# Optimization experiments

Measured on AMD Instinct MI355X. Metric: run time of the kernel, lower is better.

## Reference

```python
import jax, jax.numpy as jnp
import numpy as np
import math

B, C_IN, S, E, H, DFF = 8, 16, 1024, 128, 8, 512
DH = E // H
EPS_BN = 1e-5
EPS_LN = 1e-5


def _tape_pe(d_model, seq_len):
    pos = jnp.arange(seq_len, dtype=jnp.float32)[:, None]
    div = jnp.exp(jnp.arange(0, d_model, 2, dtype=jnp.float32) * (-math.log(10000.0) / d_model))
    ang = pos * div * (d_model / seq_len)
    pe = jnp.zeros((seq_len, d_model), dtype=jnp.float32)
    pe = pe.at[:, 0::2].set(jnp.sin(ang))
    pe = pe.at[:, 1::2].set(jnp.cos(ang))
    return pe  # [S, E]


def _ln(x, g, b, eps=EPS_LN):
    m = jnp.mean(x, axis=-1, keepdims=True)
    v = jnp.mean((x - m) ** 2, axis=-1, keepdims=True)
    return (x - m) / jnp.sqrt(v + eps) * g + b


def _bn(x, g, b, mean, var, eps=EPS_BN):
    # eval-mode BatchNorm2d over channel axis 1 of NCHW
    sh = (1, -1, 1, 1)
    return (x - mean.reshape(sh)) / jnp.sqrt(var.reshape(sh) + eps) * g.reshape(sh) + b.reshape(sh)


def setup_inputs() -> dict:
    key = jax.random.key(0)
    ks = jax.random.split(key, 24)
    f = lambda k, shape, s=0.05: (jax.random.normal(k, shape, dtype=jnp.float32) * s)
    inp = {
        'x': jax.random.normal(ks[0], (B, C_IN, S), dtype=jnp.float32),
        'conv1_w': f(ks[1], (E * 4, 1, 1, 7)),
        'conv1_b': f(ks[2], (E * 4,)),
        'bn1_g': 1.0 + f(ks[3], (E * 4,)),
        'bn1_b': f(ks[4], (E * 4,)),
        'bn1_m': jnp.zeros((E * 4,), jnp.float32),
        'bn1_v': jnp.ones((E * 4,), jnp.float32),
        'conv2_w': f(ks[5], (E, E * 4, C_IN, 1)),
        'conv2_b': f(ks[6], (E,)),
        'bn2_g': 1.0 + f(ks[7], (E,)),
        'bn2_b': f(ks[8], (E,)),
        'bn2_m': jnp.zeros((E,), jnp.float32),
        'bn2_v': jnp.ones((E,), jnp.float32),
        'wq': f(ks[9], (E, E)),
        'wk': f(ks[10], (E, E)),
        'wv': f(ks[11], (E, E)),
        'rel_bias_table': f(ks[12], (2 * S - 1, H), 0.02),
        'ln_attn_g': jnp.ones((E,), jnp.float32),
        'ln_attn_b': jnp.zeros((E,), jnp.float32),
        'ln1_g': jnp.ones((E,), jnp.float32),
        'ln1_b': jnp.zeros((E,), jnp.float32),
        'ln2_g': jnp.ones((E,), jnp.float32),
        'ln2_b': jnp.zeros((E,), jnp.float32),
        'ff_w1': f(ks[13], (DFF, E)),
        'ff_b1': f(ks[14], (DFF,)),
        'ff_w2': f(ks[15], (E, DFF)),
        'ff_b2': f(ks[16], (E,)),
    }
    return inp


def reference(x, conv1_w, conv1_b, bn1_g, bn1_b, bn1_m, bn1_v,
              conv2_w, conv2_b, bn2_g, bn2_b, bn2_m, bn2_v,
              wq, wk, wv, rel_bias_table,
              ln_attn_g, ln_attn_b, ln1_g, ln1_b, ln2_g, ln2_b,
              ff_w1, ff_b1, ff_w2, ff_b2):
    dn = ('NCHW', 'OIHW', 'NCHW')
    # conv stem: x [B, C_in, S] -> [B, 1, C_in, S]
    h = x[:, None, :, :]
    h = jax.lax.conv_general_dilated(h, conv1_w, (1, 1), [(0, 0), (3, 3)], dimension_numbers=dn)
    h = h + conv1_b[None, :, None, None]
    h = jax.nn.gelu(_bn(h, bn1_g, bn1_b, bn1_m, bn1_v), approximate=False)
    h = jax.lax.conv_general_dilated(h, conv2_w, (1, 1), [(0, 0), (0, 0)], dimension_numbers=dn)
    h = h + conv2_b[None, :, None, None]
    h = jax.nn.gelu(_bn(h, bn2_g, bn2_b, bn2_m, bn2_v), approximate=False)
    x_src = jnp.transpose(h[:, :, 0, :], (0, 2, 1))  # [B, S, E]

    # tAPE absolute positional encoding
    x_pos = x_src + _tape_pe(E, S)[None]

    # Attention_Rel_Scl (eRPE): bias added AFTER softmax, as in the original
    scale = E ** (-0.5)
    q = jnp.einsum('bsd,ed->bse', x_pos, wq).reshape(B, S, H, DH).transpose(0, 2, 1, 3)
    k = jnp.einsum('bsd,ed->bse', x_pos, wk).reshape(B, S, H, DH).transpose(0, 2, 1, 3)
    v = jnp.einsum('bsd,ed->bse', x_pos, wv).reshape(B, S, H, DH).transpose(0, 2, 1, 3)
    attn = jax.nn.softmax(jnp.einsum('bhid,bhjd->bhij', q, k) * scale, axis=-1)
    idx = jnp.arange(S)[:, None] - jnp.arange(S)[None, :] + (S - 1)  # [S, S]
    rel_bias = rel_bias_table[idx].transpose(2, 0, 1)[None]  # [1, H, S, S]
    attn = attn + rel_bias
    out = jnp.einsum('bhij,bhjd->bhid', attn, v).transpose(0, 2, 1, 3).reshape(B, S, E)
    out = _ln(out, ln_attn_g, ln_attn_b)

    att = _ln(x_src + out, ln1_g, ln1_b)
    ff = jnp.maximum(jnp.einsum('bsd,fd->bsf', att, ff_w1) + ff_b1, 0.0)
    ff = jnp.einsum('bsf,ef->bse', ff, ff_w2) + ff_b2
    y = _ln(att + ff, ln2_g, ln2_b)
    return jnp.transpose(y, (0, 2, 1))  # [B, E, S]
```

## Files before the change

kernel.cpp:

```cpp
#include <hip/hip_runtime.h>
#include <math.h>

#define BB    8
#define CIN   16
#define SS    1024
#define EE    128
#define HH    8
#define DHH   16
#define O1    512
#define DFFN  512
#define K2TOT 8192

#define PE_OFF    0
#define BN1SC_OFF 131072
#define BN1SH_OFF 131584
#define BN2SC_OFF 132096
#define BN2SH_OFF 132224
#define W1P_OFF   133120
#define WQKV_BF_OFF 135168
#define W1FF_BF_OFF 159744
#define W2FF_BF_OFF 192512
#define XSRC_OFF  262144
#define Q_OFF     1310720
#define KK_OFF    2359296
#define V_OFF     3407872
#define ATTN_OFF  4456448
#define ATT_OFF   5505024
#define FFH_OFF   6553600
#define W2CONV_BF_OFF 8650752

typedef __attribute__((ext_vector_type(8))) short short8;
typedef __attribute__((ext_vector_type(8))) unsigned short ushort8;
typedef __attribute__((ext_vector_type(4))) unsigned short us4;
typedef __attribute__((ext_vector_type(4))) float f32x4;
typedef _Float16 f16_t;
typedef __attribute__((ext_vector_type(4))) _Float16 half4;
typedef __attribute__((ext_vector_type(8))) _Float16 half8;

__device__ __forceinline__ float wave_sum(float v) {
    #pragma unroll
    for (int o = 32; o > 0; o >>= 1) v += __shfl_xor(v, o);
    return v;
}

__device__ __forceinline__ float gelu_exact(float x) {
    return 0.5f * x * (1.0f + erff(x * 0.7071067811865476f));
}

__device__ __forceinline__ float gelu_tanh(float x) {
    float x2 = x * x;
    float y = x * fmaf(0.0713548162f, x2, 1.5957691216f);
    float E = __expf(y);
    float r = __builtin_amdgcn_rcpf(E + 1.0f);
    return fmaf(-x, r, x);
}

__device__ __forceinline__ unsigned short f2bf(float f) {
    unsigned int u = __float_as_uint(f);
    unsigned int r = u + 0x7FFFu + ((u >> 16) & 1u);
    return (unsigned short)(r >> 16);
}

__device__ __forceinline__ float bf2f(unsigned short u) {
    return __uint_as_float(((unsigned int)u) << 16);
}

__device__ __forceinline__ void castw_body(const float* __restrict__ src,
                                           unsigned short* __restrict__ dst, int K, int tid) {
    int g = tid & 7, e = (tid >> 3) & 127, rest = tid >> 10;
    int KB = K >> 6;
    int kb = rest % KB, nb = rest / KB;
    int col = nb * 128 + e;
    const float* s = src + (size_t)col * K + kb * 64 + ((g ^ (e & 7)) << 3);
    ushort8 v;
    #pragma unroll
    for (int j = 0; j < 8; j++) v[j] = f2bf(s[j]);
    *(ushort8*)&dst[(size_t)tid << 3] = v;
}

__global__ __launch_bounds__(256) void k0_all(const float* __restrict__ conv1_w,
                                              const float* __restrict__ conv1_b,
                                              const float* __restrict__ bn1_g,
                                              const float* __restrict__ bn1_b,
                                              const float* __restrict__ bn1_m,
                                              const float* __restrict__ bn1_v,
                                              const float* __restrict__ conv2_w,
                                              const float* __restrict__ conv2_b,
                                              const float* __restrict__ bn2_g,
                                              const float* __restrict__ bn2_b,
                                              const float* __restrict__ bn2_m,
                                              const float* __restrict__ bn2_v,
                                              const float* __restrict__ wq,
                                              const float* __restrict__ wk,
                                              const float* __restrict__ wv,
                                              const float* __restrict__ ff_w1,
                                              const float* __restrict__ ff_w2,
                                              float* __restrict__ ws) {
    int bid = blockIdx.x, t = threadIdx.x;
    if (bid < 512) {
        int idx = bid * 256 + t;
        int s = idx >> 7, e = idx & 127;
        int i = e >> 1;
        float freq = expf((float)(2 * i) * (-9.210340371976184f / 128.0f));
        float ang = (float)s * freq * 0.125f;
        ws[PE_OFF + idx] = (e & 1) ? cosf(ang) : sinf(ang);
    } else if (bid < 515) {
        int u = (bid - 512) * 256 + t;
        if (u < 512) {
            float sc = bn1_g[u] * rsqrtf(bn1_v[u] + 1e-5f);
            ws[BN1SC_OFF + u] = sc;
            ws[BN1SH_OFF + u] = (conv1_b[u] - bn1_m[u]) * sc + bn1_b[u];
        } else if (u < 640) {
            int e = u - 512;
            float sc = bn2_g[e] * rsqrtf(bn2_v[e] + 1e-5f);
            ws[BN2SC_OFF + e] = sc;
            ws[BN2SH_OFF + e] = (conv2_b[e] - bn2_m[e]) * sc + bn2_b[e];
        }
    } else if (bid < 1027) {
        castw_body(conv2_w, (unsigned short*)(ws + W2CONV_BF_OFF), 8192, (bid - 515) * 256 + t);
    } else if (bid < 1035) {
        castw_body(wq, (unsigned short*)(ws + WQKV_BF_OFF), 128, (bid - 1027) * 256 + t);
    } else if (bid < 1043) {
        castw_body(wk, (unsigned short*)(ws + WQKV_BF_OFF) + 16384, 128, (bid - 1035) * 256 + t);
    } else if (bid < 1051) {
        castw_body(wv, (unsigned short*)(ws + WQKV_BF_OFF) + 32768, 128, (bid - 1043) * 256 + t);
    } else if (bid < 1083) {
        castw_body(ff_w1, (unsigned short*)(ws + W1FF_BF_OFF), 128, (bid - 1051) * 256 + t);
    } else if (bid < 1115) {
        castw_body(ff_w2, (unsigned short*)(ws + W2FF_BF_OFF), 512, (bid - 1083) * 256 + t);
    } else {
        unsigned short* w1p = (unsigned short*)(ws + W1P_OFF);
        for (int id = t; id < 4096; id += 256) {
            int o = id >> 3, u = id & 7;
            float sc = bn1_g[o] * rsqrtf(bn1_v[o] + 1e-5f);
            float v = (u < 7) ? conv1_w[o * 7 + u] * sc : 0.f;
            w1p[id] = f2bf(v);
        }
    }
}

__global__ __launch_bounds__(256, 3) void k1_mfma(const float* __restrict__ x,
                                                  float* __restrict__ ws) {
    __shared__ float xt[CIN][40];
    __shared__ unsigned short w1ps[256 * 8];
    __shared__ float sh1s[256];
    __shared__ unsigned short Ab[2][32 * 64];

    const int t = threadIdx.x;
    const int wave = t >> 6, lane = t & 63;
    const int row0 = blockIdx.x * 32;
    const int ksplit = blockIdx.y;
    const int b = row0 >> 10, s0 = row0 & 1023;
    const int obase = ksplit * 256;

    for (int i = t; i < CIN * 38; i += 256) {
        int c = i / 38, j = i % 38;
        int gs = s0 + j - 3;
        xt[c][j] = (gs >= 0 && gs < SS) ? x[(b * CIN + c) * SS + gs] : 0.f;
    }
    {
        const ushort8* w1pg = (const ushort8*)((const unsigned short*)(ws + W1P_OFF)) + obase;
        if (t < 256) *(ushort8*)&w1ps[t << 3] = w1pg[t];
        if (t < 256) sh1s[t] = ws[BN1SH_OFF + obase + t];
    }
    __syncthreads();

    const char* w2g = (const char*)(ws + W2CONV_BF_OFF);
    const int wr = wave >> 1, wc = wave & 1;
    const int lrow = lane & 15, lq = lane >> 4;

    int boff[8];
    #pragma unroll
    for (int ks2 = 0; ks2 < 2; ++ks2) {
        int G = (ks2 << 2) + lq;
        #pragma unroll
        for (int nf = 0; nf < 4; ++nf) {
            int e = (wc << 6) + (nf << 4) + lrow;
            boff[ks2 * 4 + nf] = (e << 7) + ((G ^ (e & 7)) << 4);
        }
    }

    auto loadB = [&](int kbl, short8 (&dst)[8]) {
        const char* g = w2g + ((size_t)(ksplit * 64 + kbl) << 14);
        #pragma unroll
        for (int i = 0; i < 8; ++i)
            dst[i] = *(const short8*)(g + boff[i]);
    };

    const int c_ = lane & 15;
    float xv[14];
    #pragma unroll
    for (int j = 0; j < 14; j++) xv[j] = xt[c_][(wave << 3) + j];
    int wbase[8];
    #pragma unroll
    for (int i = 0; i < 8; i++) {
        int ss = (wave << 3) + i;
        wbase[i] = (ss << 6) + ((((lane >> 3) ^ (ss & 7))) << 3) + (lane & 7);
    }

    auto computeH1 = [&](int kbl, int buf) {
        int ol = (kbl << 2) + (lane >> 4);
        ushort8 wv8 = *(const ushort8*)&w1ps[ol << 3];
        float w0 = bf2f(wv8[0]), w1_ = bf2f(wv8[1]), w2_ = bf2f(wv8[2]), w3 = bf2f(wv8[3]);
        float w4 = bf2f(wv8[4]), w5 = bf2f(wv8[5]), w6 = bf2f(wv8[6]);
        float sh = sh1s[ol];
        unsigned short* abf = &Ab[buf][0];
        #pragma unroll
        for (int i = 0; i < 8; i++) {
            float p = xv[i]   * w0 + xv[i+1] * w1_ + xv[i+2] * w2_ + xv[i+3] * w3
                    + xv[i+4] * w4 + xv[i+5] * w5 + xv[i+6] * w6;
            abf[wbase[i]] = f2bf(gelu_tanh(p + sh));
        }
    };

    f32x4 acc[4];
    #pragma unroll
    for (int i = 0; i < 4; i++) acc[i] = (f32x4){0.f, 0.f, 0.f, 0.f};

    auto mfmaPhase = [&](short8 (&bb)[8], int buf) {
        #pragma unroll
        for (int ks2 = 0; ks2 < 2; ++ks2) {
            int G = (ks2 << 2) + lq;
            int arow = (wr << 4) + lrow;
            short8 a = *(const short8*)&Ab[buf][(arow << 6) + ((G ^ (arow & 7)) << 3)];
            #pragma unroll
            for (int nf = 0; nf < 4; ++nf)
                acc[nf] = __builtin_amdgcn_mfma_f32_16x16x32_bf16(a, bb[ks2 * 4 + nf], acc[nf], 0, 0, 0);
        }
    };

    short8 bA[8], bB[8];
    loadB(0, bA);
    computeH1(0, 0);
    __syncthreads();
    for (int kb2 = 0; kb2 < 64; kb2 += 2) {
        loadB(kb2 + 1, bB);
        mfmaPhase(bA, 0);
        computeH1(kb2 + 1, 1);
        __syncthreads();
        if (kb2 + 2 < 64) loadB(kb2 + 2, bA);
        mfmaPhase(bB, 1);
        if (kb2 + 2 < 64) {
            computeH1(kb2 + 2, 0);
            __syncthreads();
        }
    }

    float* P = ws + FFH_OFF + (size_t)ksplit * 1048576;
    #pragma unroll
    for (int nf = 0; nf < 4; ++nf) {
        int e = (wc << 6) + (nf << 4) + lrow;
        #pragma unroll
        for (int r = 0; r < 4; ++r) {
            int srow = s0 + (wr << 4) + (lq << 2) + r;
            P[(((size_t)(b * SS + srow)) << 7) + e] = acc[nf][r];
        }
    }
}

__global__ __launch_bounds__(256) void k1b_combine(float* __restrict__ ws) {
    int f = (blockIdx.x * 256 + threadIdx.x) * 4;
    int e0 = f & 127;
    float4 p0 = *(const float4*)&ws[FFH_OFF + f];
    float4 p1 = *(const float4*)&ws[FFH_OFF + 1048576 + f];
    float4 sc = *(const float4*)&ws[BN2SC_OFF + e0];
    float4 sh = *(const float4*)&ws[BN2SH_OFF + e0];
    float4 o;
    o.x = gelu_exact(fmaf(p0.x + p1.x, sc.x, sh.x));
    o.y = gelu_exact(fmaf(p0.y + p1.y, sc.y, sh.y));
    o.z = gelu_exact(fmaf(p0.z + p1.z, sc.z, sh.z));
    o.w = gelu_exact(fmaf(p0.w + p1.w, sc.w, sh.w));
    *(float4*)&ws[XSRC_OFF + f] = o;
}

__global__ __launch_bounds__(256) void k2_mfma(float* __restrict__ ws) {
    __shared__ unsigned short As[32 * 128];
    __shared__ unsigned short Bs[128 * 128];
    __shared__ float ys[32][132];
    const int t = threadIdx.x;
    const int rt = blockIdx.x, mat = blockIdx.y;
    const int wave = t >> 6, lane = t & 63;

    const char* bg = (const char*)((const unsigned short*)(ws + WQKV_BF_OFF) + mat * 16384);
    #pragma unroll
    for (int c8 = 0; c8 < 8; ++c8) {
        int off = c8 * 4096 + wave * 1024;
        __builtin_amdgcn_global_load_lds(
            (const __attribute__((address_space(1))) unsigned int*)(bg + off + lane * 16),
            (__attribute__((address_space(3))) unsigned int*)(&Bs[off >> 1]), 16, 0, 0);
    }
    const int bs0 = rt * 32;
    const int sl0 = bs0 & 1023;
    for (int i = t; i < 1024; i += 256) {
        int row = i >> 5, d0 = (i & 31) << 2;
        float4 xvv = *(const float4*)&ws[XSRC_OFF + (size_t)(bs0 + row) * EE + d0];
        float4 pv = *(const float4*)&ws[PE_OFF + (size_t)(sl0 + row) * EE + d0];
        us4 o;
        o[0] = f2bf(xvv.x + pv.x); o[1] = f2bf(xvv.y + pv.y);
        o[2] = f2bf(xvv.z + pv.z); o[3] = f2bf(xvv.w + pv.w);
        int slot = (d0 >> 3) ^ (row & 7);
        *(us4*)&As[(row << 7) + (slot << 3) + (d0 & 7)] = o;
    }
    __syncthreads();

    const int wr = wave >> 1, wc = wave & 1;
    const int lrow = lane & 15, lq = lane >> 4;
    f32x4 acc[4];
    #pragma unroll
    for (int i = 0; i < 4; i++) acc[i] = (f32x4){0.f, 0.f, 0.f, 0.f};

    #pragma unroll
    for (int ksname = 0; ksname < 4; ++ksname) {
        int G = (ksname << 2) + lq;
        int arow = (wr << 4) + lrow;
        short8 a = *(const short8*)&As[(arow << 7) + ((G ^ (arow & 7)) << 3)];
        #pragma unroll
        for (int nf = 0; nf < 4; ++nf) {
            int e = (wc << 6) + (nf << 4) + lrow;
            short8 bf = *(const short8*)&Bs[((G >> 3) << 13) + (e << 6) + (((G & 7) ^ (e & 7)) << 3)];
            acc[nf] = __builtin_amdgcn_mfma_f32_16x16x32_bf16(a, bf, acc[nf], 0, 0, 0);
        }
    }

    #pragma unroll
    for (int nf = 0; nf < 4; ++nf) {
        int e = (wc << 6) + (nf << 4) + lrow;
        #pragma unroll
        for (int r = 0; r < 4; ++r)
            ys[(wr << 4) + (lq << 2) + r][e] = acc[nf][r];
    }
    __syncthreads();

    const int b = bs0 >> 10;
    if (mat <= 1) {
        int row = t >> 3, h8 = t & 7;
        float scl = (mat == 0) ? 0.08838834764831845f : 1.0f;
        f16_t* dst = (f16_t*)(ws + (mat == 0 ? Q_OFF : KK_OFF))
                   + (((size_t)(b * HH + h8)) * SS + (sl0 + row)) * DHH;
        half8 v0, v1;
        #pragma unroll
        for (int d = 0; d < 8; d++) v0[d] = (f16_t)(ys[row][h8 * 16 + d] * scl);
        #pragma unroll
        for (int d = 0; d < 8; d++) v1[d] = (f16_t)(ys[row][h8 * 16 + 8 + d] * scl);
        *(half8*)&dst[0] = v0;
        *(half8*)&dst[8] = v1;
    } else {
        int c = t & 127, hf = t >> 7;
        int h8 = c >> 4, d2 = c & 15;
        f16_t* dst = (f16_t*)(ws + V_OFF)
                   + (((size_t)(b * HH + h8)) * DHH + d2) * SS + sl0 + hf * 16;
        half8 v0, v1;
        #pragma unroll
        for (int r = 0; r < 8; r++) v0[r] = (f16_t)ys[hf * 16 + r][c];
        #pragma unroll
        for (int r = 0; r < 8; r++) v1[r] = (f16_t)ys[hf * 16 + 8 + r][c];
        *(half8*)&dst[0] = v0;
        *(half8*)&dst[8] = v1;
    }
}

__global__ __launch_bounds__(256) void k3_attn(const float* __restrict__ rel_tab,
                                               float* __restrict__ ws) {
    __shared__ f16_t rtbl4[4][1088];
    const int bh = blockIdx.x;
    const int h = bh & 7, b = bh >> 3;
    const int i0b = blockIdx.y * 64;
    const int t = threadIdx.x;
    for (int id = t; id < 4 * 1088; id += 256) {
        int p = id / 1088; int j = id - p * 1088;
        int u = j + p;
        float v = (u < 1087) ? rel_tab[(i0b + 1086 - u) * HH + h] : 0.f;
        rtbl4[p][j] = (f16_t)v;
    }
    __syncthreads();

    const int w = t >> 6, lane = t & 63;
    const int q = lane & 15, g = lane >> 4;
    const int r = w * 16 + q;
    const int i = i0b + r;

    const f16_t* QH  = (const f16_t*)(ws + Q_OFF)  + (size_t)bh * SS * DHH;
    const f16_t* KH  = (const f16_t*)(ws + KK_OFF) + (size_t)bh * SS * DHH;
    const f16_t* VHT = (const f16_t*)(ws + V_OFF)  + (size_t)bh * DHH * SS;

    half4 qf = *(const half4*)&QH[(size_t)i * DHH + 4 * g];
    f32x4 o = {0.f, 0.f, 0.f, 0.f};
    f32x4 bv = {0.f, 0.f, 0.f, 0.f};
    const f32x4 zf = {0.f, 0.f, 0.f, 0.f};
    float lp = 0.f;
    const int p4 = (63 - r + 4 * g) & 3;

    #pragma unroll 4
    for (int jt = 0; jt < 64; ++jt) {
        half4 kf = *(const half4*)&KH[(size_t)(jt * 16 + q) * DHH + 4 * g];
        f32x4 s = __builtin_amdgcn_mfma_f32_16x16x16f16(kf, qf, zf, 0, 0, 0);
        float p0 = __expf(s[0]), p1 = __expf(s[1]), p2 = __expf(s[2]), p3 = __expf(s[3]);
        lp += (p0 + p1) + (p2 + p3);
        half4 pf;
        pf[0] = (f16_t)p0; pf[1] = (f16_t)p1; pf[2] = (f16_t)p2; pf[3] = (f16_t)p3;
        half4 vf = *(const half4*)&VHT[(size_t)q * SS + jt * 16 + 4 * g];
        o = __builtin_amdgcn_mfma_f32_16x16x16f16(vf, pf, o, 0, 0, 0);
        int vb = 63 - r + jt * 16 + 4 * g;
        half4 bfrag = *(const half4*)&rtbl4[p4][vb & ~3];
        bv = __builtin_amdgcn_mfma_f32_16x16x16f16(vf, bfrag, bv, 0, 0, 0);
    }
    lp += __shfl_xor(lp, 16);
    lp += __shfl_xor(lp, 32);
    float inv = 1.f / lp;
    float4 ov = make_float4(fmaf(o[0], inv, bv[0]), fmaf(o[1], inv, bv[1]),
                            fmaf(o[2], inv, bv[2]), fmaf(o[3], inv, bv[3]));
    *(float4*)&ws[ATTN_OFF + ((size_t)(b * SS) + i) * EE + h * DHH + 4 * g] = ov;
}

__global__ __launch_bounds__(256) void k4_ln(const float* __restrict__ g_attn, const float* __restrict__ b_attn,
                                             const float* __restrict__ g1, const float* __restrict__ b1,
                                             float* __restrict__ ws) {
    int row = blockIdx.x * 4 + (threadIdx.x >> 6);
    int lane = threadIdx.x & 63;
    int e0 = lane * 2;
    const float* ain = ws + ATTN_OFF + (size_t)row * EE;
    const float* xsr = ws + XSRC_OFF + (size_t)row * EE;
    float2 a = *(const float2*)(ain + e0);
    float mean = wave_sum(a.x + a.y) * (1.f / 128.f);
    float dx = a.x - mean, dy = a.y - mean;
    float var = wave_sum(dx * dx + dy * dy) * (1.f / 128.f);
    float inv = rsqrtf(var + 1e-5f);
    float n0 = dx * inv * g_attn[e0] + b_attn[e0];
    float n1 = dy * inv * g_attn[e0 + 1] + b_attn[e0 + 1];
    float2 xs2 = *(const float2*)(xsr + e0);
    float z0 = xs2.x + n0, z1 = xs2.y + n1;
    float m2 = wave_sum(z0 + z1) * (1.f / 128.f);
    float d0 = z0 - m2, d1 = z1 - m2;
    float v2 = wave_sum(d0 * d0 + d1 * d1) * (1.f / 128.f);
    float inv2 = rsqrtf(v2 + 1e-5f);
    float o0 = d0 * inv2 * g1[e0] + b1[e0];
    float o1 = d1 * inv2 * g1[e0 + 1] + b1[e0 + 1];
    *(float2*)(ws + ATT_OFF + (size_t)row * EE + e0) = make_float2(o0, o1);
}

__global__ __launch_bounds__(256) void k5_mfma(const float* __restrict__ b1,
                                               float* __restrict__ ws) {
    __shared__ unsigned short As[32 * 128];
    __shared__ unsigned short Bs[128 * 128];
    __shared__ float ys[32][132];
    const int t = threadIdx.x;
    const int rt = blockIdx.x, nb = blockIdx.y;
    const int wave = t >> 6, lane = t & 63;

    const char* bg = (const char*)((const unsigned short*)(ws + W1FF_BF_OFF) + nb * 16384);
    #pragma unroll
    for (int c8 = 0; c8 < 8; ++c8) {
        int off = c8 * 4096 + wave * 1024;
        __builtin_amdgcn_global_load_lds(
            (const __attribute__((address_space(1))) unsigned int*)(bg + off + lane * 16),
            (__attribute__((address_space(3))) unsigned int*)(&Bs[off >> 1]), 16, 0, 0);
    }
    const int bs0 = rt * 32;
    for (int i = t; i < 1024; i += 256) {
        int row = i >> 5, d0 = (i & 31) << 2;
        float4 xvv = *(const float4*)&ws[ATT_OFF + (size_t)(bs0 + row) * EE + d0];
        us4 o;
        o[0] = f2bf(xvv.x); o[1] = f2bf(xvv.y); o[2] = f2bf(xvv.z); o[3] = f2bf(xvv.w);
        int slot = (d0 >> 3) ^ (row & 7);
        *(us4*)&As[(row << 7) + (slot << 3) + (d0 & 7)] = o;
    }
    __syncthreads();

    const int wr = wave >> 1, wc = wave & 1;
    const int lrow = lane & 15, lq = lane >> 4;
    f32x4 acc[4];
    #pragma unroll
    for (int i = 0; i < 4; i++) acc[i] = (f32x4){0.f, 0.f, 0.f, 0.f};

    #pragma unroll
    for (int ksname = 0; ksname < 4; ++ksname) {
        int G = (ksname << 2) + lq;
        int arow = (wr << 4) + lrow;
        short8 a = *(const short8*)&As[(arow << 7) + ((G ^ (arow & 7)) << 3)];
        #pragma unroll
        for (int nf = 0; nf < 4; ++nf) {
            int e = (wc << 6) + (nf << 4) + lrow;
            short8 bf = *(const short8*)&Bs[((G >> 3) << 13) + (e << 6) + (((G & 7) ^ (e & 7)) << 3)];
            acc[nf] = __builtin_amdgcn_mfma_f32_16x16x32_bf16(a, bf, acc[nf], 0, 0, 0);
        }
    }

    #pragma unroll
    for (int nf = 0; nf < 4; ++nf) {
        int col = (wc << 6) + (nf << 4) + lrow;
        float bias = b1[(nb << 7) + col];
        #pragma unroll
        for (int r = 0; r < 4; ++r)
            ys[(wr << 4) + (lq << 2) + r][col] = fmaxf(acc[nf][r] + bias, 0.f);
    }
    __syncthreads();

    unsigned short* ffhb = (unsigned short*)(ws + FFH_OFF);
    #pragma unroll
    for (int kk = 0; kk < 2; ++kk) {
        int id = t + kk * 256;
        int ssr = id >> 4, fg = id & 15;
        float4 v0 = *(const float4*)&ys[ssr][fg * 8];
        float4 v1 = *(const float4*)&ys[ssr][fg * 8 + 4];
        ushort8 ov;
        ov[0] = f2bf(v0.x); ov[1] = f2bf(v0.y); ov[2] = f2bf(v0.z); ov[3] = f2bf(v0.w);
        ov[4] = f2bf(v1.x); ov[5] = f2bf(v1.y); ov[6] = f2bf(v1.z); ov[7] = f2bf(v1.w);
        int kb = (nb << 1) + (fg >> 3);
        int slot = (fg & 7) ^ (ssr & 7);
        *(ushort8*)&ffhb[(((size_t)(rt * 8 + kb) * 32 + ssr) << 6) + (slot << 3)] = ov;
    }
}

__global__ __launch_bounds__(256) void k6_mfma(const float* __restrict__ b2,
                                               const float* __restrict__ g2, const float* __restrict__ bb2,
                                               float* __restrict__ ws, float* __restrict__ out) {
    __shared__ unsigned short Ab[2][2048];
    __shared__ unsigned short Bb[2][8192];
    __shared__ float y[32][132];
    const int t = threadIdx.x;
    const int wave = t >> 6, lane = t & 63;
    const int rt = blockIdx.x;

    const char* ag = (const char*)((const unsigned short*)(ws + FFH_OFF) + (size_t)rt * 16384);
    const char* bgc = (const char*)(ws + W2FF_BF_OFF);

    auto stage = [&](int kb, int buf) {
        __builtin_amdgcn_global_load_lds(
            (const __attribute__((address_space(1))) unsigned int*)(ag + kb * 4096 + t * 16),
            (__attribute__((address_space(3))) unsigned int*)(&Ab[buf][(t * 16) >> 1]), 16, 0, 0);
        const char* g = bgc + kb * 16384;
        #pragma unroll
        for (int c4 = 0; c4 < 4; ++c4) {
            int off = c4 * 4096 + wave * 1024;
            __builtin_amdgcn_global_load_lds(
                (const __attribute__((address_space(1))) unsigned int*)(g + off + lane * 16),
                (__attribute__((address_space(3))) unsigned int*)(&Bb[buf][off >> 1]), 16, 0, 0);
        }
    };

    const int wr = wave >> 1, wc = wave & 1;
    const int lrow = lane & 15, lq = lane >> 4;
    f32x4 acc[4];
    #pragma unroll
    for (int i = 0; i < 4; i++) acc[i] = (f32x4){0.f, 0.f, 0.f, 0.f};

    stage(0, 0);
    __syncthreads();
    for (int kb = 0; kb < 8; ++kb) {
        int cur = kb & 1;
        if (kb < 7) stage(kb + 1, cur ^ 1);
        #pragma unroll
        for (int ksname = 0; ksname < 2; ++ksname) {
            int G = (ksname << 2) + lq;
            int arow = (wr << 4) + lrow;
            short8 a = *(const short8*)&Ab[cur][(arow << 6) + ((G ^ (arow & 7)) << 3)];
            #pragma unroll
            for (int nf = 0; nf < 4; ++nf) {
                int e = (wc << 6) + (nf << 4) + lrow;
                short8 bf = *(const short8*)&Bb[cur][(e << 6) + ((G ^ (e & 7)) << 3)];
                acc[nf] = __builtin_amdgcn_mfma_f32_16x16x32_bf16(a, bf, acc[nf], 0, 0, 0);
            }
        }
        __syncthreads();
    }

    const int bs0 = rt * 32;
    #pragma unroll
    for (int nf = 0; nf < 4; ++nf) {
        int e = (wc << 6) + (nf << 4) + lrow;
        float bvv = b2[e];
        #pragma unroll
        for (int r = 0; r < 4; ++r) {
            int row = (wr << 4) + (lq << 2) + r;
            y[row][e] = acc[nf][r] + bvv + ws[ATT_OFF + (size_t)(bs0 + row) * EE + e];
        }
    }
    __syncthreads();
    int e0 = lane * 2;
    for (int rr = 0; rr < 8; rr++) {
        int row = wave * 8 + rr;
        float z0 = y[row][e0], z1 = y[row][e0 + 1];
        float mean = wave_sum(z0 + z1) * (1.f / 128.f);
        float d0 = z0 - mean, d1 = z1 - mean;
        float var = wave_sum(d0 * d0 + d1 * d1) * (1.f / 128.f);
        float inv = rsqrtf(var + 1e-5f);
        y[row][e0]     = d0 * inv * g2[e0] + bb2[e0];
        y[row][e0 + 1] = d1 * inv * g2[e0 + 1] + bb2[e0 + 1];
    }
    __syncthreads();
    int b = bs0 >> 10, s0 = bs0 & 1023;
    int sl = t & 31, eg = t >> 5;
    #pragma unroll
    for (int rep = 0; rep < 16; rep++) {
        int e = eg * 16 + rep;
        out[(size_t)b * EE * SS + (size_t)e * SS + s0 + sl] = y[sl][e];
    }
}

extern "C" void kernel_launch(void* const* d_in, const int* in_sizes, int n_in,
                              void* d_out, int out_size, void* d_ws, size_t ws_size,
                              hipStream_t stream) {
    const float* x        = (const float*)d_in[0];
    const float* conv1_w  = (const float*)d_in[1];
    const float* conv1_b  = (const float*)d_in[2];
    const float* bn1_g    = (const float*)d_in[3];
    const float* bn1_b    = (const float*)d_in[4];
    const float* bn1_m    = (const float*)d_in[5];
    const float* bn1_v    = (const float*)d_in[6];
    const float* conv2_w  = (const float*)d_in[7];
    const float* conv2_b  = (const float*)d_in[8];
    const float* bn2_g    = (const float*)d_in[9];
    const float* bn2_b    = (const float*)d_in[10];
    const float* bn2_m    = (const float*)d_in[11];
    const float* bn2_v    = (const float*)d_in[12];
    const float* wq       = (const float*)d_in[13];
    const float* wk       = (const float*)d_in[14];
    const float* wv       = (const float*)d_in[15];
    const float* rel_tab  = (const float*)d_in[16];
    const float* ln_attn_g = (const float*)d_in[17];
    const float* ln_attn_b = (const float*)d_in[18];
    const float* ln1_g    = (const float*)d_in[19];
    const float* ln1_b    = (const float*)d_in[20];
    const float* ln2_g    = (const float*)d_in[21];
    const float* ln2_b    = (const float*)d_in[22];
    const float* ff_w1    = (const float*)d_in[23];
    const float* ff_b1    = (const float*)d_in[24];
    const float* ff_w2    = (const float*)d_in[25];
    const float* ff_b2    = (const float*)d_in[26];

    float* ws  = (float*)d_ws;
    float* out = (float*)d_out;

    hipLaunchKernelGGL(k0_all, dim3(1116), dim3(256), 0, stream,
                       conv1_w, conv1_b, bn1_g, bn1_b, bn1_m, bn1_v,
                       conv2_w, conv2_b, bn2_g, bn2_b, bn2_m, bn2_v,
                       wq, wk, wv, ff_w1, ff_w2, ws);
    hipLaunchKernelGGL(k1_mfma, dim3(256, 2), dim3(256), 0, stream, x, ws);
    hipLaunchKernelGGL(k1b_combine, dim3(1024), dim3(256), 0, stream, ws);
    hipLaunchKernelGGL(k2_mfma, dim3(256, 3), dim3(256), 0, stream, ws);
    hipLaunchKernelGGL(k3_attn, dim3(BB * HH, SS / 64), dim3(256), 0, stream, rel_tab, ws);
    hipLaunchKernelGGL(k4_ln, dim3(BB * SS / 4), dim3(256), 0, stream, ln_attn_g, ln_attn_b, ln1_g, ln1_b, ws);
    hipLaunchKernelGGL(k5_mfma, dim3(256, 4), dim3(256), 0, stream, ff_b1, ws);
    hipLaunchKernelGGL(k6_mfma, dim3(256), dim3(256), 0, stream, ff_b2, ln2_g, ln2_b, ws, out);
}
```

Before: 168.0 us.

## Compute conv1 A-fragments in registers and split K four ways in k1

The fused conv1+conv2 kernel no longer stages GELU'd conv1 outputs through double-buffered shared memory. Each lane now computes its bf16 MFMA A-fragment directly in registers from a preloaded 56-value x window. Tiles grow to 64 rows by 128 columns per block, and the reduction is split four ways instead of two. The four partial results go into the otherwise-unused Q/K/V/ATTN buffers and are summed in the combine kernel. This removes the LDS round-trip and the barriers from the main loop. In exchange it costs more registers, drops the explicit prefetch pipeline, and adds extra partial-sum traffic in the combine step.

```diff
diff --git a/kernel.cpp b/kernel.cpp
--- a/kernel.cpp
+++ b/kernel.cpp
@@ -139,120 +139,102 @@
     }
 }
 
-__global__ __launch_bounds__(256, 3) void k1_mfma(const float* __restrict__ x,
-                                                  float* __restrict__ ws) {
-    __shared__ float xt[CIN][40];
-    __shared__ unsigned short w1ps[256 * 8];
-    __shared__ float sh1s[256];
-    __shared__ unsigned short Ab[2][32 * 64];
+__global__ __launch_bounds__(256) void k1_mfma(const float* __restrict__ x,
+                                               float* __restrict__ ws) {
+    __shared__ float xt[CIN][72];
+    __shared__ unsigned short w1ps[128 * 8];
+    __shared__ float sh1s[128];
 
     const int t = threadIdx.x;
     const int wave = t >> 6, lane = t & 63;
-    const int row0 = blockIdx.x * 32;
+    const int row0 = blockIdx.x * 64;
     const int ksplit = blockIdx.y;
     const int b = row0 >> 10, s0 = row0 & 1023;
-    const int obase = ksplit * 256;
-
-    for (int i = t; i < CIN * 38; i += 256) {
-        int c = i / 38, j = i % 38;
+    const int obase = ksplit * 128;
+
+    for (int i = t; i < CIN * 70; i += 256) {
+        int c = i / 70, j = i % 70;
         int gs = s0 + j - 3;
         xt[c][j] = (gs >= 0 && gs < SS) ? x[(b * CIN + c) * SS + gs] : 0.f;
     }
-    {
-        const ushort8* w1pg = (const ushort8*)((const unsigned short*)(ws + W1P_OFF)) + obase;
-        if (t < 256) *(ushort8*)&w1ps[t << 3] = w1pg[t];
-        if (t < 256) sh1s[t] = ws[BN1SH_OFF + obase + t];
-    }
-    __syncthreads();
-
-    const char* w2g = (const char*)(ws + W2CONV_BF_OFF);
-    const int wr = wave >> 1, wc = wave & 1;
+    if (t < 128) {
+        *(ushort8*)&w1ps[t << 3] =
+            ((const ushort8*)((const unsigned short*)(ws + W1P_OFF)))[obase + t];
+        sh1s[t] = ws[BN1SH_OFF + obase + t];
+    }
+    __syncthreads();
+
     const int lrow = lane & 15, lq = lane >> 4;
-
-    int boff[8];
+    const int srow_local = (wave << 4) + lrow;
+    const int cbase = (lq & 1) << 3;
+
+    float xv[56];
+    #pragma unroll
+    for (int c8 = 0; c8 < 8; ++c8)
+        #pragma unroll
+        for (int u = 0; u < 7; ++u)
+            xv[c8 * 7 + u] = xt[cbase + c8][srow_local + u];
+
+    int boff[16];
     #pragma unroll
     for (int ks2 = 0; ks2 < 2; ++ks2) {
         int G = (ks2 << 2) + lq;
         #pragma unroll
-        for (int nf = 0; nf < 4; ++nf) {
-            int e = (wc << 6) + (nf << 4) + lrow;
-            boff[ks2 * 4 + nf] = (e << 7) + ((G ^ (e & 7)) << 4);
-        }
-    }
-
-    auto loadB = [&](int kbl, short8 (&dst)[8]) {
-        const char* g = w2g + ((size_t)(ksplit * 64 + kbl) << 14);
-        #pragma unroll
-        for (int i = 0; i < 8; ++i)
-            dst[i] = *(const short8*)(g + boff[i]);
+        for (int nf = 0; nf < 8; ++nf) {
+            int e = (nf << 4) + lrow;
+            boff[ks2 * 8 + nf] = (e << 7) + ((G ^ (e & 7)) << 4);
+        }
+    }
+
+    const char* w2g = (const char*)(ws + W2CONV_BF_OFF);
+    const int olq = lq >> 1;
+
+    auto computeA = [&](int kbl, int ks2) -> short8 {
+        int ol = (kbl << 2) + (ks2 << 1) + olq;
+        ushort8 w8 = *(const ushort8*)&w1ps[ol << 3];
+        float w0 = bf2f(w8[0]), w1_ = bf2f(w8[1]), w2_ = bf2f(w8[2]), w3 = bf2f(w8[3]);
+        float w4 = bf2f(w8[4]), w5 = bf2f(w8[5]), w6 = bf2f(w8[6]);
+        float sh = sh1s[ol];
+        short8 a;
+        #pragma unroll
+        for (int j = 0; j < 8; ++j) {
+            float p = xv[j*7]   * w0 + xv[j*7+1] * w1_ + xv[j*7+2] * w2_ + xv[j*7+3] * w3
+                    + xv[j*7+4] * w4 + xv[j*7+5] * w5 + xv[j*7+6] * w6;
+            a[j] = (short)f2bf(gelu_tanh(p + sh));
+        }
+        return a;
     };
 
-    const int c_ = lane & 15;
-    float xv[14];
-    #pragma unroll
-    for (int j = 0; j < 14; j++) xv[j] = xt[c_][(wave << 3) + j];
-    int wbase[8];
-    #pragma unroll
-    for (int i = 0; i < 8; i++) {
-        int ss = (wave << 3) + i;
-        wbase[i] = (ss << 6) + ((((lane >> 3) ^ (ss & 7))) << 3) + (lane & 7);
-    }
-
-    auto computeH1 = [&](int kbl, int buf) {
-        int ol = (kbl << 2) + (lane >> 4);
-        ushort8 wv8 = *(const ushort8*)&w1ps[ol << 3];
-        float w0 = bf2f(wv8[0]), w1_ = bf2f(wv8[1]), w2_ = bf2f(wv8[2]), w3 = bf2f(wv8[3]);
-        float w4 = bf2f(wv8[4]), w5 = bf2f(wv8[5]), w6 = bf2f(wv8[6]);
-        float sh = sh1s[ol];
-        unsigned short* abf = &Ab[buf][0];
-        #pragma unroll
-        for (int i = 0; i < 8; i++) {
-            float p = xv[i]   * w0 + xv[i+1] * w1_ + xv[i+2] * w2_ + xv[i+3] * w3
-                    + xv[i+4] * w4 + xv[i+5] * w5 + xv[i+6] * w6;
-            abf[wbase[i]] = f2bf(gelu_tanh(p + sh));
-        }
-    };
-
-    f32x4 acc[4];
-    #pragma unroll
-    for (int i = 0; i < 4; i++) acc[i] = (f32x4){0.f, 0.f, 0.f, 0.f};
-
-    auto mfmaPhase = [&](short8 (&bb)[8], int buf) {
-        #pragma unroll
-        for (int ks2 = 0; ks2 < 2; ++ks2) {
-            int G = (ks2 << 2) + lq;
-            int arow = (wr << 4) + lrow;
-            short8 a = *(const short8*)&Ab[buf][(arow << 6) + ((G ^ (arow & 7)) << 3)];
-            #pragma unroll
-            for (int nf = 0; nf < 4; ++nf)
-                acc[nf] = __builtin_amdgcn_mfma_f32_16x16x32_bf16(a, bb[ks2 * 4 + nf], acc[nf], 0, 0, 0);
-        }
-    };
-
-    short8 bA[8], bB[8];
-    loadB(0, bA);
-    computeH1(0, 0);
-    __syncthreads();
-    for (int kb2 = 0; kb2 < 64; kb2 += 2) {
-        loadB(kb2 + 1, bB);
-        mfmaPhase(bA, 0);
-        computeH1(kb2 + 1, 1);
-        __syncthreads();
-        if (kb2 + 2 < 64) loadB(kb2 + 2, bA);
-        mfmaPhase(bB, 1);
-        if (kb2 + 2 < 64) {
-            computeH1(kb2 + 2, 0);
-            __syncthreads();
-        }
-    }
-
-    float* P = ws + FFH_OFF + (size_t)ksplit * 1048576;
-    #pragma unroll
-    for (int nf = 0; nf < 4; ++nf) {
-        int e = (wc << 6) + (nf << 4) + lrow;
+    f32x4 acc[8];
+    #pragma unroll
+    for (int i = 0; i < 8; ++i) acc[i] = (f32x4){0.f, 0.f, 0.f, 0.f};
+
+    #pragma unroll 1
+    for (int kbl = 0; kbl < 32; ++kbl) {
+        const char* g = w2g + ((size_t)((ksplit << 5) + kbl) << 14);
+        short8 bA_[8];
+        #pragma unroll
+        for (int i = 0; i < 8; ++i) bA_[i] = *(const short8*)(g + boff[i]);
+        short8 a0 = computeA(kbl, 0);
+        short8 bB_[8];
+        #pragma unroll
+        for (int i = 0; i < 8; ++i) bB_[i] = *(const short8*)(g + boff[8 + i]);
+        #pragma unroll
+        for (int nf = 0; nf < 8; ++nf)
+            acc[nf] = __builtin_amdgcn_mfma_f32_16x16x32_bf16(a0, bA_[nf], acc[nf], 0, 0, 0);
+        short8 a1 = computeA(kbl, 1);
+        #pragma unroll
+        for (int nf = 0; nf < 8; ++nf)
+            acc[nf] = __builtin_amdgcn_mfma_f32_16x16x32_bf16(a1, bB_[nf], acc[nf], 0, 0, 0);
+    }
+
+    float* P = ws + Q_OFF + (size_t)ksplit * 1048576;
+    #pragma unroll
+    for (int nf = 0; nf < 8; ++nf) {
+        int e = (nf << 4) + lrow;
         #pragma unroll
         for (int r = 0; r < 4; ++r) {
-            int srow = s0 + (wr << 4) + (lq << 2) + r;
+            int srow = s0 + (wave << 4) + (lq << 2) + r;
             P[(((size_t)(b * SS + srow)) << 7) + e] = acc[nf][r];
         }
     }
@@ -261,15 +243,17 @@
 __global__ __launch_bounds__(256) void k1b_combine(float* __restrict__ ws) {
     int f = (blockIdx.x * 256 + threadIdx.x) * 4;
     int e0 = f & 127;
-    float4 p0 = *(const float4*)&ws[FFH_OFF + f];
-    float4 p1 = *(const float4*)&ws[FFH_OFF + 1048576 + f];
+    float4 p0 = *(const float4*)&ws[Q_OFF + f];
+    float4 p1 = *(const float4*)&ws[KK_OFF + f];
+    float4 p2 = *(const float4*)&ws[V_OFF + f];
+    float4 p3 = *(const float4*)&ws[ATTN_OFF + f];
     float4 sc = *(const float4*)&ws[BN2SC_OFF + e0];
     float4 sh = *(const float4*)&ws[BN2SH_OFF + e0];
     float4 o;
-    o.x = gelu_exact(fmaf(p0.x + p1.x, sc.x, sh.x));
-    o.y = gelu_exact(fmaf(p0.y + p1.y, sc.y, sh.y));
-    o.z = gelu_exact(fmaf(p0.z + p1.z, sc.z, sh.z));
-    o.w = gelu_exact(fmaf(p0.w + p1.w, sc.w, sh.w));
+    o.x = gelu_exact(fmaf((p0.x + p1.x) + (p2.x + p3.x), sc.x, sh.x));
+    o.y = gelu_exact(fmaf((p0.y + p1.y) + (p2.y + p3.y), sc.y, sh.y));
+    o.z = gelu_exact(fmaf((p0.z + p1.z) + (p2.z + p3.z), sc.z, sh.z));
+    o.w = gelu_exact(fmaf((p0.w + p1.w) + (p2.w + p3.w), sc.w, sh.w));
     *(float4*)&ws[XSRC_OFF + f] = o;
 }
 
@@ -635,7 +619,7 @@
                        conv1_w, conv1_b, bn1_g, bn1_b, bn1_m, bn1_v,
                        conv2_w, conv2_b, bn2_g, bn2_b, bn2_m, bn2_v,
                        wq, wk, wv, ff_w1, ff_w2, ws);
-    hipLaunchKernelGGL(k1_mfma, dim3(256, 2), dim3(256), 0, stream, x, ws);
+    hipLaunchKernelGGL(k1_mfma, dim3(128, 4), dim3(256), 0, stream, x, ws);
     hipLaunchKernelGGL(k1b_combine, dim3(1024), dim3(256), 0, stream, ws);
     hipLaunchKernelGGL(k2_mfma, dim3(256, 3), dim3(256), 0, stream, ws);
     hipLaunchKernelGGL(k3_attn, dim3(BB * HH, SS / 64), dim3(256), 0, stream, rel_tab, ws);
```

New measurement: 157.8 us (median of 2 runs). -6.0%, faster.
